# Optimization experiments

Measured on AMD Instinct MI355X. Metric: run time of the kernel, lower is better.

Reference implementation:

```python
import jax, jax.numpy as jnp
import numpy as np

V, E, H, NL, B, T = 32000, 256, 256, 2, 32, 256


def setup_inputs() -> dict:
    key = jax.random.key(0)
    ks = jax.random.split(key, 20)
    s = 0.05
    d = {}
    d['x'] = jax.random.randint(ks[0], (B, T), 0, V)
    d['encoder_output'] = jax.random.normal(ks[1], (T + 1, B, 2 * H), jnp.float32)
    d['encoder_final_state'] = jax.random.normal(ks[2], (2 * NL, B, H), jnp.float32)
    d['embedding'] = jax.random.normal(ks[3], (V, E), jnp.float32) * s
    d['enc_proj_w'] = jax.random.normal(ks[4], (H, 2 * H), jnp.float32) * s
    d['enc_proj_b'] = jnp.zeros((H,), jnp.float32)
    d['attn_wq'] = jax.random.normal(ks[5], (H, H), jnp.float32) * s
    d['attn_wk'] = jax.random.normal(ks[6], (H, H), jnp.float32) * s
    d['attn_wv'] = jax.random.normal(ks[7], (H,), jnp.float32) * s
    d['gru_w_ih0'] = jax.random.normal(ks[8], (3 * H, E + H), jnp.float32) * s
    d['gru_w_hh0'] = jax.random.normal(ks[9], (3 * H, H), jnp.float32) * s
    d['gru_b_ih0'] = jnp.zeros((3 * H,), jnp.float32)
    d['gru_b_hh0'] = jnp.zeros((3 * H,), jnp.float32)
    d['gru_w_ih1'] = jax.random.normal(ks[10], (3 * H, H), jnp.float32) * s
    d['gru_w_hh1'] = jax.random.normal(ks[11], (3 * H, H), jnp.float32) * s
    d['gru_b_ih1'] = jnp.zeros((3 * H,), jnp.float32)
    d['gru_b_hh1'] = jnp.zeros((3 * H,), jnp.float32)
    d['dense_w'] = jax.random.normal(ks[12], (V, H), jnp.float32) * s
    d['dense_b'] = jnp.zeros((V,), jnp.float32)
    return d


def _gru_cell(xin, h, w_ih, w_hh, b_ih, b_hh):
    gi = xin @ w_ih.T + b_ih
    gh = h @ w_hh.T + b_hh
    i_r, i_z, i_n = jnp.split(gi, 3, axis=-1)
    h_r, h_z, h_n = jnp.split(gh, 3, axis=-1)
    r = jax.nn.sigmoid(i_r + h_r)
    z = jax.nn.sigmoid(i_z + h_z)
    n = jnp.tanh(i_n + r * h_n)
    return (1.0 - z) * n + z * h


def _forward(x, encoder_output, encoder_final_state, embedding, enc_proj_w, enc_proj_b,
             attn_wq, attn_wk, attn_wv,
             gru_w_ih0, gru_w_hh0, gru_b_ih0, gru_b_hh0,
             gru_w_ih1, gru_w_hh1, gru_b_ih1, gru_b_hh1,
             dense_w, dense_b):
    Bb, Tt = x.shape
    Hh = enc_proj_w.shape[0]
    L = 2 * Tt  # fixed KV buffer length (= max attention width)
    # project encoder output: (B, T+1, H)
    proj = jnp.einsum('sbd,hd->bsh', encoder_output, enc_proj_w) + enc_proj_b
    # sum forward/backward encoder final states -> (n_layers, B, H)
    h0 = encoder_final_state.reshape(NL, 2, Bb, Hh).sum(axis=1)
    emb = embedding[x].transpose(1, 0, 2)  # (T, B, E)
    # fixed-size KV buffer; slots [0, T+1) hold projected encoder output
    kv0 = jnp.zeros((Bb, L, Hh), proj.dtype).at[:, :Tt + 1, :].set(proj)
    kproj0 = jnp.einsum('blh,gh->blg', kv0, attn_wk)  # precomputed key projections

    def step(carry, inp):
        h, kv, kproj = carry
        emb_t, t = inp
        q = h[-1] @ attn_wq.T  # (B, H)
        scores = jnp.tanh(kproj + q[:, None, :]) @ attn_wv  # (B, L)
        valid = jnp.arange(L) < (Tt + 1 + t)
        attn = jax.nn.softmax(jnp.where(valid[None, :], scores, -1e9), axis=-1)
        attn = attn * valid[None, :].astype(attn.dtype)  # exact zeros at padding
        context = jnp.einsum('bl,blh->bh', attn, kv)
        xin = jnp.concatenate([context, emb_t], axis=-1)  # (B, H+E)
        h0n = _gru_cell(xin, h[0], gru_w_ih0, gru_w_hh0, gru_b_ih0, gru_b_hh0)
        h1n = _gru_cell(h0n, h[1], gru_w_ih1, gru_w_hh1, gru_b_ih1, gru_b_hh1)
        h_new = jnp.stack([h0n, h1n], axis=0)
        out = h1n  # top-layer output for this timestep
        pos = Tt + 1 + t
        kv = jax.lax.dynamic_update_slice_in_dim(kv, out[:, None, :], pos, axis=1)
        kproj = jax.lax.dynamic_update_slice_in_dim(kproj, (out @ attn_wk.T)[:, None, :], pos, axis=1)
        return (h_new, kv, kproj), (out, attn)

    (_, _, _), (outs, attns) = jax.lax.scan(step, (h0, kv0, kproj0), (emb, jnp.arange(Tt)))
    outs = outs.transpose(1, 0, 2)  # (B, T, H)
    logits = jnp.einsum('bth,vh->btv', outs, dense_w) + dense_b  # (B, T, V)
    attn_scores = attns.transpose(1, 0, 2)  # (B, T, 2T)
    return logits, attn_scores


def reference(x, encoder_output, encoder_final_state, embedding, enc_proj_w, enc_proj_b,
              attn_wq, attn_wk, attn_wv,
              gru_w_ih0, gru_w_hh0, gru_b_ih0, gru_b_hh0,
              gru_w_ih1, gru_w_hh1, gru_b_ih1, gru_b_hh1,
              dense_w, dense_b):
    return _forward(x, encoder_output, encoder_final_state, embedding, enc_proj_w, enc_proj_b,
                    attn_wq, attn_wk, attn_wv,
                    gru_w_ih0, gru_w_hh0, gru_b_ih0, gru_b_hh0,
                    gru_w_ih1, gru_w_hh1, gru_b_ih1, gru_b_hh1,
                    dense_w, dense_b)
```

## Files before the change

kernel.cpp:

```cpp
#include <hip/hip_runtime.h>
#include <hip/hip_bf16.h>
#include <hip/hip_fp16.h>

#define NB 32
#define NT 256
#define NH 256
#define NV 32000
#define NL2 512
#define NTP1 257

typedef unsigned int u32x4 __attribute__((ext_vector_type(4)));
typedef unsigned int u32x2 __attribute__((ext_vector_type(2)));
typedef short s16x8 __attribute__((ext_vector_type(8)));
typedef float f32x4 __attribute__((ext_vector_type(4)));
typedef _Float16 half2v __attribute__((ext_vector_type(2)));

#define AGENT __HIP_MEMORY_SCOPE_AGENT
__device__ __forceinline__ float aload(const float* p) {
  return __hip_atomic_load((float*)p, __ATOMIC_RELAXED, AGENT);
}
__device__ __forceinline__ void astore(float* p, float v) {
  __hip_atomic_store(p, v, __ATOMIC_RELAXED, AGENT);
}

__device__ __forceinline__ float dot2f(half2v a, half2v b, float c) {
#if __has_builtin(__builtin_amdgcn_fdot2)
  return __builtin_amdgcn_fdot2(a, b, c, false);
#else
  return c + (float)a[0] * (float)b[0] + (float)a[1] * (float)b[1];
#endif
}
__device__ __forceinline__ half2v h2(unsigned int u) { return __builtin_bit_cast(half2v, u); }

__device__ __forceinline__ float dot16h(const _Float16* __restrict__ w,
                                        const _Float16* __restrict__ x) {
  u32x4 a0 = *(const u32x4*)w;
  u32x4 a1 = *(const u32x4*)(w + 8);
  u32x4 b0 = *(const u32x4*)x;
  u32x4 b1 = *(const u32x4*)(x + 8);
  float acc = 0.f;
  acc = dot2f(h2(a0.x), h2(b0.x), acc);
  acc = dot2f(h2(a0.y), h2(b0.y), acc);
  acc = dot2f(h2(a0.z), h2(b0.z), acc);
  acc = dot2f(h2(a0.w), h2(b0.w), acc);
  acc = dot2f(h2(a1.x), h2(b1.x), acc);
  acc = dot2f(h2(a1.y), h2(b1.y), acc);
  acc = dot2f(h2(a1.z), h2(b1.z), acc);
  acc = dot2f(h2(a1.w), h2(b1.w), acc);
  return acc;
}

__device__ __forceinline__ float fast_tanh(float x) {
  x = fminf(15.f, fmaxf(-15.f, x));
  float e = __expf(2.f * x);
  return 1.f - __fdividef(2.f, e + 1.f);
}
__device__ __forceinline__ float fast_sigmoid(float x) {
  x = fminf(30.f, fmaxf(-30.f, x));
  float e = __expf(-x);
  return __fdividef(1.f, 1.f + e);
}
__device__ __forceinline__ unsigned short f2bf(float f) {
  unsigned int u = __builtin_bit_cast(unsigned int, f);
  return (unsigned short)((u + 0x7FFFu + ((u >> 16) & 1u)) >> 16);
}

__device__ __forceinline__ void batch_barrier(int* __restrict__ ctr, int target) {
  __syncthreads();
  if (threadIdx.x == 0) {
    __hip_atomic_fetch_add(ctr, 1, __ATOMIC_RELEASE, AGENT);
    while (__hip_atomic_load(ctr, __ATOMIC_RELAXED, AGENT) < target)
      __builtin_amdgcn_s_sleep(1);
    asm volatile("" ::: "memory");
  }
  __syncthreads();
}


__global__ void conv_f16_kernel(const float* __restrict__ s, _Float16* __restrict__ d, int n) {
  int i = blockIdx.x * 256 + threadIdx.x;
  if (i < n) d[i] = (_Float16)s[i];
}

__global__ void conv_bf16_kernel(const float* __restrict__ s, unsigned short* __restrict__ d, int n) {
  int i = blockIdx.x * 256 + threadIdx.x;
  if (i < n) d[i] = f2bf(s[i]);
}

__global__ void packT_kernel(const float* __restrict__ w, unsigned int* __restrict__ out,
                             int R, int K) {
  int gid = blockIdx.x * 256 + threadIdx.x;
  int K2 = K >> 1;
  if (gid >= R * K2) return;
  int k2 = gid / R, r = gid - k2 * R;
  unsigned short ua = __builtin_bit_cast(unsigned short, (_Float16)w[(size_t)r * K + 2 * k2]);
  unsigned short ub = __builtin_bit_cast(unsigned short, (_Float16)w[(size_t)r * K + 2 * k2 + 1]);
  out[(size_t)k2 * R + r] = (unsigned int)ua | ((unsigned int)ub << 16);
}

__global__ void transpose_kernel(const float* __restrict__ w, float* __restrict__ wT) {
  int i = blockIdx.x * 256 + threadIdx.x;
  if (i < 256 * 512) { int h = i >> 9, dd = i & 511; wT[dd * 256 + h] = w[i]; }
}
// ... 48 lines not shown
      float kvv = (float)kvL[((size_t)b * 512 + l) * 256 + h];
#pragma unroll
      for (int g = 0; g < 32; ++g) acc[g] = fmaf(kvv, wks[g][h], acc[g]);
    }
    for (int g = 0; g < 32; ++g)
      kprojL[((size_t)b * NL2 + l) * NH + gq * 32 + g] = (_Float16)acc[g];
  }
  {
    int g = tid >> 3, hc = tid & 7;
    float acc = 0.f;
    for (int h = hc * 32; h < hc * 32 + 32; ++h)
      acc += (float)kvL[((size_t)b * 512 + 256) * 256 + h] * wks[g][h];
    pk[g][hc] = acc;
    __syncthreads();
    if (tid < 32) {
      float sv = 0.f;
      for (int c = 0; c < 8; ++c) sv += pk[tid][c];
      kprojL[((size_t)b * NL2 + 256) * NH + gq * 32 + tid] = (_Float16)sv;
    }
  }
}


__global__ __launch_bounds__(512) void scan_kernel(
    const int* __restrict__ x, const float* __restrict__ efs, const float* __restrict__ emb,
    const float* __restrict__ wv,
    const float* __restrict__ bih0, const float* __restrict__ bhh0,
    const float* __restrict__ bih1, const float* __restrict__ bhh1,
    const _Float16* __restrict__ wq16, const _Float16* __restrict__ wk16,
    const unsigned int* __restrict__ wih0T, const unsigned int* __restrict__ whh0T,
    const unsigned int* __restrict__ wih1T, const unsigned int* __restrict__ whh1T,
    const unsigned int* __restrict__ kvL_u, const unsigned int* __restrict__ kprojL_u,
    float* __restrict__ spart, float* __restrict__ vec0, float* __restrict__ vec1,
    int* __restrict__ bars,
    unsigned short* __restrict__ outs_bf, float* __restrict__ attn_out) {
  __shared__ __align__(16) unsigned int kp_u[512 * 17];
  __shared__ __align__(16) unsigned int kv_u[512 * 19];
  __shared__ __align__(16) float att[512], gsum[1024];
  __shared__ __align__(16) float h0s[256], h1s[256];
  __shared__ __align__(16) float scr[544], scr2[32 * 35];
  __shared__ __align__(16) float qs[32], wvs[32], red[16];
  __shared__ __align__(16) _Float16 h0h[256], h1h[256], xinh[64];

  int tid = threadIdx.x;
  int b = blockIdx.x & 31;
  int s = blockIdx.x >> 5;
  int* bar = bars + b * 32;

  if (tid < 256) {
    float h0v = efs[(size_t)(0 * NB + b) * NH + tid] + efs[(size_t)(1 * NB + b) * NH + tid];
    float h1v = efs[(size_t)(2 * NB + b) * NH + tid] + efs[(size_t)(3 * NB + b) * NH + tid];
    h0s[tid] = h0v; h0h[tid] = (_Float16)h0v;
    h1s[tid] = h1v; h1h[tid] = (_Float16)h1v;
  }
  if (tid < 32) wvs[tid] = wv[32 * s + tid];
  for (int idx = tid; idx < 257 * 16; idx += 512) {
    int l = idx >> 4, c = idx & 15;
    kp_u[l * 17 + c] = kprojL_u[((size_t)b * 512 + l) * 128 + 16 * s + c];
    kv_u[l * 19 + c] = kvL_u[((size_t)b * 512 + l) * 128 + 16 * s + c];
  }
  for (int idx = tid; idx < 255 * 16; idx += 512) {
    int l = 257 + (idx >> 4), c = idx & 15;
    kp_u[l * 17 + c] = 0u;
    kv_u[l * 19 + c] = 0u;
  }
  __syncthreads();

  for (int t = 0; t < NT; ++t) {
    int Lt = NTP1 + t;
    int tgt = 8 * (t + 1);
    {
      int row = tid & 31, ch = tid >> 5;
      scr[ch * 33 + row] = dot16h(wq16 + (size_t)(32 * s + row) * 256 + ch * 16, h1h + ch * 16);
      if (tid >= 480) {
        int j = tid - 480;
        int tok = x[b * NT + t];
        xinh[32 + j] = (_Float16)emb[(size_t)tok * 256 + 32 * s + j];
      }
    }
    __syncthreads();
    if (tid < 32) {
      float a = 0.f;
#pragma unroll
      for (int c = 0; c < 16; ++c) a += scr[c * 33 + tid];
      qs[tid] = a;
    }
    __syncthreads();
    {
      float acc = 0.f;
      if (tid < Lt) {
        const unsigned int* kr = kp_u + tid * 17;
#pragma unroll 4
        for (int g2 = 0; g2 < 16; ++g2) {
          half2v kp2 = h2(kr[g2]);
          acc = fmaf(wvs[2 * g2 + 0], fast_tanh((float)kp2[0] + qs[2 * g2 + 0]), acc);
          acc = fmaf(wvs[2 * g2 + 1], fast_tanh((float)kp2[1] + qs[2 * g2 + 1]), acc);
        }
      }
      astore(spart + ((size_t)(b * 8 + s)) * 512 + tid, acc);
    }
    batch_barrier(bar + 0, tgt);
    {
      float sum = 0.f;
#pragma unroll
      for (int sp = 0; sp < 8; ++sp) sum += aload(spart + ((size_t)(b * 8 + sp)) * 512 + tid);
      float v = (tid < Lt) ? sum : -3.0e38f;
      float m = v;
#pragma unroll
      for (int off = 32; off; off >>= 1) m = fmaxf(m, __shfl_xor(m, off, 64));
      if ((tid & 63) == 0) red[tid >> 6] = m;
      __syncthreads();
      float M = red[0];
#pragma unroll
      for (int i = 1; i < 8; ++i) M = fmaxf(M, red[i]);
      float e = (tid < Lt) ? __expf(v - M) : 0.f;
      float zz = e;
#pragma unroll
      for (int off = 32; off; off >>= 1) zz += __shfl_xor(zz, off, 64);
      if ((tid & 63) == 0) red[8 + (tid >> 6)] = zz;
      __syncthreads();
      float Z = red[8];
#pragma unroll
      for (int i = 1; i < 8; ++i) Z += red[8 + i];
      float a = __fdividef(e, Z);
      att[tid] = a;
      if ((tid >> 6) == s) attn_out[((size_t)(b * NT + t)) * NL2 + tid] = a;
    }
    __syncthreads();
    {
      int c = tid >> 4, hh = tid & 15;
      float aA = 0.f, aB = 0.f;
#pragma unroll
      for (int j = 0; j < 16; ++j) {
        int l = 16 * c + j;
        half2v kv2 = h2(kv_u[l * 19 + hh]);
        float av = att[l];
        aA = fmaf((float)kv2[0], av, aA);
        aB = fmaf((float)kv2[1], av, aB);
      }
      scr2[c * 35 + 2 * hh] = aA;
      scr2[c * 35 + 2 * hh + 1] = aB;
    }
    __syncthreads();
    if (tid < 32) {
      float a = 0.f;
#pragma unroll
      for (int c = 0; c < 32; ++c) a += scr2[c * 35 + tid];
      xinh[tid] = (_Float16)a;
    }
    __syncthreads();
    {
      const unsigned int* xu = (const unsigned int*)xinh;
      const unsigned int* h0u = (const unsigned int*)h0h;
      float accA = 0.f, accI = 0.f, accH = 0.f;
      bool dual = (tid < 256);
#pragma unroll 2
      for (int i = 0; i < 16; ++i) {
        unsigned int xc = xu[i], xe = xu[16 + i];
        const unsigned int* wc = wih0T + (size_t)(16 * s + i) * 768;
        const unsigned int* we = wih0T + (size_t)(128 + 16 * s + i) * 768;
        accA = dot2f(h2(wc[tid]), h2(xc), accA);
        accA = dot2f(h2(we[tid]), h2(xe), accA);
        if (dual) {
          accI = dot2f(h2(wc[512 + tid]), h2(xc), accI);
          accI = dot2f(h2(we[512 + tid]), h2(xe), accI);
        }
      }
#pragma unroll 2
      for (int i = 0; i < 16; ++i) {
        unsigned int hv = h0u[16 * s + i];
        const unsigned int* wr = whh0T + (size_t)(16 * s + i) * 768;
        accA = dot2f(h2(wr[tid]), h2(hv), accA);
        if (dual) accH = dot2f(h2(wr[512 + tid]), h2(hv), accH);
      }
      float* vb = vec0 + (size_t)(b * 8 + s) * 1024;
      astore(vb + tid, accA);
      if (dual) { astore(vb + 512 + tid, accI); astore(vb + 768 + tid, accH); }
    }
    batch_barrier(bar + 1, tgt);
    {
      float t0 = 0.f, t1 = 0.f;
#pragma unroll
      for (int sp = 0; sp < 8; ++sp) {
        const float* vb = vec0 + (size_t)(b * 8 + sp) * 1024;
        t0 += aload(vb + tid);
        t1 += aload(vb + 512 + tid);
      }
      gsum[tid] = t0; gsum[512 + tid] = t1;
    }
    __syncthreads();
    if (tid < 256) {
      float rr = fast_sigmoid(gsum[tid] + bih0[tid] + bhh0[tid]);
      float zz = fast_sigmoid(gsum[256 + tid] + bih0[256 + tid] + bhh0[256 + tid]);
      float nn = fast_tanh(gsum[512 + tid] + bih0[512 + tid] + rr * (gsum[768 + tid] + bhh0[512 + tid]));
      float hv = (1.f - zz) * nn + zz * h0s[tid];
      h0s[tid] = hv; h0h[tid] = (_Float16)hv;
    }
    __syncthreads();
    {
      const unsigned int* h0u = (const unsigned int*)h0h;
      const unsigned int* h1u = (const unsigned int*)h1h;
      float accA = 0.f, accI = 0.f, accH = 0.f;
      bool dual = (tid < 256);
#pragma unroll 2
      for (int i = 0; i < 16; ++i) {
        unsigned int xv = h0u[16 * s + i];
        unsigned int hv = h1u[16 * s + i];
        const unsigned int* wi = wih1T + (size_t)(16 * s + i) * 768;
        const unsigned int* wh = whh1T + (size_t)(16 * s + i) * 768;
        accA = dot2f(h2(wi[tid]), h2(xv), accA);
        accA = dot2f(h2(wh[tid]), h2(hv), accA);
        if (dual) {
          accI = dot2f(h2(wi[512 + tid]), h2(xv), accI);
          accH = dot2f(h2(wh[512 + tid]), h2(hv), accH);
        }
      }
      float* vb = vec1 + (size_t)(b * 8 + s) * 1024;
      astore(vb + tid, accA);
      if (dual) { astore(vb + 512 + tid, accI); astore(vb + 768 + tid, accH); }
    }
    batch_barrier(bar + 2, tgt);
    {
      float t0 = 0.f, t1 = 0.f;
#pragma unroll
      for (int sp = 0; sp < 8; ++sp) {
        const float* vb = vec1 + (size_t)(b * 8 + sp) * 1024;
        t0 += aload(vb + tid);
        t1 += aload(vb + 512 + tid);
      }
      gsum[tid] = t0; gsum[512 + tid] = t1;
    }
    __syncthreads();
    if (tid < 256) {
      float rr = fast_sigmoid(gsum[tid] + bih1[tid] + bhh1[tid]);
      float zz = fast_sigmoid(gsum[256 + tid] + bih1[256 + tid] + bhh1[256 + tid]);
      float nn = fast_tanh(gsum[512 + tid] + bih1[512 + tid] + rr * (gsum[768 + tid] + bhh1[512 + tid]));
      float hv = (1.f - zz) * nn + zz * h1s[tid];
      h1s[tid] = hv; h1h[tid] = (_Float16)hv;
      if ((tid >> 5) == s) outs_bf[((size_t)(b * NT + t)) * NH + tid] = f2bf(hv);
    }
    __syncthreads();
    if (t < NT - 1) {
      int pos = NTP1 + t;
      if (tid < 16) {
        unsigned short lo = __builtin_bit_cast(unsigned short, h1h[32 * s + 2 * tid]);
        unsigned short hi = __builtin_bit_cast(unsigned short, h1h[32 * s + 2 * tid + 1]);
        kv_u[pos * 19 + tid] = (unsigned int)lo | ((unsigned int)hi << 16);
      }
      {
        int row = tid & 31, ch = tid >> 5;
        scr[ch * 33 + row] = dot16h(wk16 + (size_t)(32 * s + row) * 256 + ch * 16, h1h + ch * 16);
      }
      __syncthreads();
      if (tid < 32) {
        float a = 0.f;
#pragma unroll
        for (int c = 0; c < 16; ++c) a += scr[c * 33 + tid];
        ((_Float16*)kp_u)[pos * 34 + tid] = (_Float16)a;
      }
      __syncthreads();
    }
  }
}


__global__ __launch_bounds__(256) void logits_gemm(const unsigned short* __restrict__ A,
                                                   const unsigned short* __restrict__ Bw,
                                                   const float* __restrict__ bias,
                                                   float* __restrict__ C) {
  __shared__ unsigned short As[128][88];
  __shared__ unsigned short Bs[128][88];
  int tid = threadIdx.x;
  int nt = blockIdx.x % 250, mt = blockIdx.x / 250;
  int m0 = mt * 128, n0 = nt * 128;
  int lane = tid & 63, w = tid >> 6;
  int wm = w & 1, wn = w >> 1;
  f32x4 acc[4][4];
#pragma unroll
  for (int m = 0; m < 4; ++m)
#pragma unroll
    for (int n = 0; n < 4; ++n) acc[m][n] = (f32x4)0.0f;

  int r0 = tid >> 3;
  int c0 = (tid & 7) * 8;
  for (int kt = 0; kt < 4; ++kt) {
    __syncthreads();
#pragma unroll
    for (int it = 0; it < 4; ++it) {
      int row = it * 32 + r0;
      u32x4 va = *(const u32x4*)(A + (size_t)(m0 + row) * 256 + kt * 64 + c0);
      u32x4 vb = *(const u32x4*)(Bw + (size_t)(n0 + row) * 256 + kt * 64 + c0);
      *(u32x4*)(&As[row][c0]) = va;
      *(u32x4*)(&Bs[row][c0]) = vb;
    }
// ... 35 lines not shown
  const int*   x    = (const int*)d_in[0];
  const float* enc  = (const float*)d_in[1];
  const float* efs  = (const float*)d_in[2];
  const float* emb  = (const float*)d_in[3];
  const float* epw  = (const float*)d_in[4];
  const float* epb  = (const float*)d_in[5];
  const float* wq   = (const float*)d_in[6];
  const float* wk   = (const float*)d_in[7];
  const float* wv   = (const float*)d_in[8];
  const float* wih0 = (const float*)d_in[9];
  const float* whh0 = (const float*)d_in[10];
  const float* bih0 = (const float*)d_in[11];
  const float* bhh0 = (const float*)d_in[12];
  const float* wih1 = (const float*)d_in[13];
  const float* whh1 = (const float*)d_in[14];
  const float* bih1 = (const float*)d_in[15];
  const float* bhh1 = (const float*)d_in[16];
  const float* dw   = (const float*)d_in[17];
  const float* db   = (const float*)d_in[18];

  const size_t o_alias  = 0;
  const size_t a_wq16   = 0;
  const size_t a_wk16   = a_wq16 + 131072;
  const size_t a_wih0T  = a_wk16 + 131072;
  const size_t a_whh0T  = a_wih0T + 786432;
  const size_t a_wih1T  = a_whh0T + 393216;
  const size_t a_whh1T  = a_wih1T + 393216;
  const size_t a_kvL    = a_whh1T + 393216;
  const size_t o_wT     = o_alias + 16384000;
  const size_t o_kprojL = o_wT + 524288;
  const size_t o_outs   = o_kprojL + 8388608;
  const size_t o_spart  = o_outs + 4194304;
  const size_t o_vec0   = o_spart + 524288;
  const size_t o_vec1   = o_vec0 + 1048576;
  const size_t o_bar    = o_vec1 + 1048576;
  const size_t need     = o_bar + 4096;
  if (ws_size < need) return;

  char* ws = (char*)d_ws;
  unsigned short* dwbf16 = (unsigned short*)(ws + o_alias);
  _Float16* wq16     = (_Float16*)(ws + a_wq16);
  _Float16* wk16     = (_Float16*)(ws + a_wk16);
  unsigned int* wih0T = (unsigned int*)(ws + a_wih0T);
  unsigned int* whh0T = (unsigned int*)(ws + a_whh0T);
  unsigned int* wih1T = (unsigned int*)(ws + a_wih1T);
  unsigned int* whh1T = (unsigned int*)(ws + a_whh1T);
  _Float16* kvL      = (_Float16*)(ws + a_kvL);
  float* wT          = (float*)(ws + o_wT);
  _Float16* kprojL   = (_Float16*)(ws + o_kprojL);
  unsigned short* outs_bf = (unsigned short*)(ws + o_outs);
  float* spart       = (float*)(ws + o_spart);
  float* vec0        = (float*)(ws + o_vec0);
  float* vec1        = (float*)(ws + o_vec1);
  int* bars          = (int*)(ws + o_bar);

  float* logits = (float*)d_out;
  float* attn_out = logits + (size_t)NB * NT * NV;

  hipMemsetAsync(ws + o_bar, 0, 4096, stream);

  conv_f16_kernel<<<(65536 + 255) / 256, 256, 0, stream>>>(wq, wq16, 65536);
  conv_f16_kernel<<<(65536 + 255) / 256, 256, 0, stream>>>(wk, wk16, 65536);
  packT_kernel<<<(768 * 256 + 255) / 256, 256, 0, stream>>>(wih0, wih0T, 768, 512);
  packT_kernel<<<(768 * 128 + 255) / 256, 256, 0, stream>>>(whh0, whh0T, 768, 256);
  packT_kernel<<<(768 * 128 + 255) / 256, 256, 0, stream>>>(wih1, wih1T, 768, 256);
  packT_kernel<<<(768 * 128 + 255) / 256, 256, 0, stream>>>(whh1, whh1T, 768, 256);
  transpose_kernel<<<(131072 + 255) / 256, 256, 0, stream>>>(epw, wT);

  proj_kernel<<<(NTP1 * NB * 64) / 256, 256, 0, stream>>>(enc, wT, epb, kvL);
  kproj0_kernel<<<NB * 8, 256, 0, stream>>>(kvL, wk, kprojL);

  scan_kernel<<<256, 512, 0, stream>>>(x, efs, emb, wv, bih0, bhh0, bih1, bhh1,
                                       wq16, wk16, wih0T, whh0T, wih1T, whh1T,
                                       (const unsigned int*)kvL, (const unsigned int*)kprojL,
                                       spart, vec0, vec1, bars,
                                       outs_bf, attn_out);

  conv_bf16_kernel<<<(8192000 + 255) / 256, 256, 0, stream>>>(dw, dwbf16, 8192000);

  logits_gemm<<<(NB * NT / 128) * (NV / 128), 256, 0, stream>>>(outs_bf, dwbf16, db, logits);
}
```

Before: 7.129 ms.

## Split grid barriers into arrive/wait and overlap hidden-state matvecs with barrier waits

Splits the cross-block barrier into arrive and wait phases. Independent work runs in the gap: both layers' W_hh·h matvecs after the attention-score barrier, the attention output store, and prefetching the next token's embedding. The partial-sum buffers become double-buffered by timestep parity and widened to hold separate input and hidden contributions, which avoids overwrite races now that writes move earlier. The aim is to hide barrier latency on the serial recurrence. The cost is larger workspace and more global partial loads in the reductions.

```diff
diff --git a/kernel.cpp b/kernel.cpp
--- a/kernel.cpp
+++ b/kernel.cpp
@@ -65,10 +65,13 @@
   return (unsigned short)((u + 0x7FFFu + ((u >> 16) & 1u)) >> 16);
 }
 
-__device__ __forceinline__ void batch_barrier(int* __restrict__ ctr, int target) {
+__device__ __forceinline__ void bar_arrive(int* __restrict__ ctr) {
   __syncthreads();
+  if (threadIdx.x == 0)
+    __hip_atomic_fetch_add(ctr, 1, __ATOMIC_RELEASE, AGENT);
+}
+__device__ __forceinline__ void bar_wait(int* __restrict__ ctr, int target) {
   if (threadIdx.x == 0) {
-    __hip_atomic_fetch_add(ctr, 1, __ATOMIC_RELEASE, AGENT);
     while (__hip_atomic_load(ctr, __ATOMIC_RELAXED, AGENT) < target)
       __builtin_amdgcn_s_sleep(1);
     asm volatile("" ::: "memory");
@@ -205,6 +208,11 @@
     h1s[tid] = h1v; h1h[tid] = (_Float16)h1v;
   }
   if (tid < 32) wvs[tid] = wv[32 * s + tid];
+  if (tid >= 480) {
+    int j = tid - 480;
+    int tok = x[b * NT + 0];
+    xinh[32 + j] = (_Float16)emb[(size_t)tok * 256 + 32 * s + j];
+  }
   for (int idx = tid; idx < 257 * 16; idx += 512) {
     int l = idx >> 4, c = idx & 15;
     kp_u[l * 17 + c] = kprojL_u[((size_t)b * 512 + l) * 128 + 16 * s + c];
@@ -220,14 +228,11 @@
   for (int t = 0; t < NT; ++t) {
     int Lt = NTP1 + t;
     int tgt = 8 * (t + 1);
+    int buf = t & 1;
+    const size_t vbase = ((size_t)(buf * NB + b)) * 8;
     {
       int row = tid & 31, ch = tid >> 5;
       scr[ch * 33 + row] = dot16h(wq16 + (size_t)(32 * s + row) * 256 + ch * 16, h1h + ch * 16);
-      if (tid >= 480) {
-        int j = tid - 480;
-        int tok = x[b * NT + t];
-        xinh[32 + j] = (_Float16)emb[(size_t)tok * 256 + 32 * s + j];
-      }
     }
     __syncthreads();
     if (tid < 32) {
@@ -250,7 +255,32 @@
       }
       astore(spart + ((size_t)(b * 8 + s)) * 512 + tid, acc);
     }
-    batch_barrier(bar + 0, tgt);
+    bar_arrive(bar + 0);
+    {
+      const unsigned int* h0u = (const unsigned int*)h0h;
+      const unsigned int* h1u = (const unsigned int*)h1h;
+      float a0v = 0.f, a0d = 0.f, a1v = 0.f, a1d = 0.f;
+      bool dual = (tid < 256);
+#pragma unroll 4
+      for (int i = 0; i < 16; ++i) {
+        unsigned int hv0 = h0u[16 * s + i];
+        unsigned int hv1 = h1u[16 * s + i];
+        const unsigned int* w0r = whh0T + (size_t)(16 * s + i) * 768;
+        const unsigned int* w1r = whh1T + (size_t)(16 * s + i) * 768;
+        a0v = dot2f(h2(w0r[tid]), h2(hv0), a0v);
+        a1v = dot2f(h2(w1r[tid]), h2(hv1), a1v);
+        if (dual) {
+          a0d = dot2f(h2(w0r[512 + tid]), h2(hv0), a0d);
+          a1d = dot2f(h2(w1r[512 + tid]), h2(hv1), a1d);
+        }
+      }
+      float* v0 = vec0 + (vbase + s) * 1536 + 768;
+      float* v1 = vec1 + (vbase + s) * 1536 + 768;
+      astore(v0 + tid, a0v);
+      astore(v1 + tid, a1v);
+      if (dual) { astore(v0 + 512 + tid, a0d); astore(v1 + 512 + tid, a1d); }
+    }
+    bar_wait(bar + 0, tgt);
     {
       float sum = 0.f;
 #pragma unroll
@@ -273,9 +303,7 @@
       float Z = red[8];
 #pragma unroll
       for (int i = 1; i < 8; ++i) Z += red[8 + i];
-      float a = __fdividef(e, Z);
-      att[tid] = a;
-      if ((tid >> 6) == s) attn_out[((size_t)(b * NT + t)) * NL2 + tid] = a;
+      att[tid] = __fdividef(e, Z);
     }
     __syncthreads();
     {
@@ -302,42 +330,47 @@
     __syncthreads();
     {
       const unsigned int* xu = (const unsigned int*)xinh;
-      const unsigned int* h0u = (const unsigned int*)h0h;
-      float accA = 0.f, accI = 0.f, accH = 0.f;
+      float g1 = 0.f, g2 = 0.f;
       bool dual = (tid < 256);
-#pragma unroll 2
+#pragma unroll 4
       for (int i = 0; i < 16; ++i) {
         unsigned int xc = xu[i], xe = xu[16 + i];
         const unsigned int* wc = wih0T + (size_t)(16 * s + i) * 768;
         const unsigned int* we = wih0T + (size_t)(128 + 16 * s + i) * 768;
-        accA = dot2f(h2(wc[tid]), h2(xc), accA);
-        accA = dot2f(h2(we[tid]), h2(xe), accA);
+        g1 = dot2f(h2(wc[tid]), h2(xc), g1);
+        g1 = dot2f(h2(we[tid]), h2(xe), g1);
         if (dual) {
-          accI = dot2f(h2(wc[512 + tid]), h2(xc), accI);
-          accI = dot2f(h2(we[512 + tid]), h2(xe), accI);
+          g2 = dot2f(h2(wc[512 + tid]), h2(xc), g2);
+          g2 = dot2f(h2(we[512 + tid]), h2(xe), g2);
         }
       }
-#pragma unroll 2
-      for (int i = 0; i < 16; ++i) {
-        unsigned int hv = h0u[16 * s + i];
-        const unsigned int* wr = whh0T + (size_t)(16 * s + i) * 768;
-        accA = dot2f(h2(wr[tid]), h2(hv), accA);
-        if (dual) accH = dot2f(h2(wr[512 + tid]), h2(hv), accH);
-      }
-      float* vb = vec0 + (size_t)(b * 8 + s) * 1024;
-      astore(vb + tid, accA);
-      if (dual) { astore(vb + 512 + tid, accI); astore(vb + 768 + tid, accH); }
-    }
-    batch_barrier(bar + 1, tgt);
-    {
-      float t0 = 0.f, t1 = 0.f;
+      float* vb = vec0 + (vbase + s) * 1536;
+      astore(vb + tid, g1);
+      if (dual) astore(vb + 512 + tid, g2);
+    }
+    bar_arrive(bar + 1);
+    if ((tid >> 6) == s) attn_out[((size_t)(b * NT + t)) * NL2 + tid] = att[tid];
+    bar_wait(bar + 1, tgt);
+    {
+      float t0 = 0.f;
 #pragma unroll
       for (int sp = 0; sp < 8; ++sp) {
-        const float* vb = vec0 + (size_t)(b * 8 + sp) * 1024;
-        t0 += aload(vb + tid);
-        t1 += aload(vb + 512 + tid);
-      }
-      gsum[tid] = t0; gsum[512 + tid] = t1;
+        const float* vb = vec0 + (vbase + sp) * 1536;
+        t0 += aload(vb + tid) + aload(vb + 768 + tid);
+      }
+      gsum[tid] = t0;
+      if (tid < 256) {
+        float ti = 0.f;
+#pragma unroll
+        for (int sp = 0; sp < 8; ++sp) ti += aload(vec0 + (vbase + sp) * 1536 + 512 + tid);
+        gsum[512 + tid] = ti;
+      } else {
+        int j = tid - 256;
+        float th = 0.f;
+#pragma unroll
+        for (int sp = 0; sp < 8; ++sp) th += aload(vec0 + (vbase + sp) * 1536 + 1280 + j);
+        gsum[768 + j] = th;
+      }
     }
     __syncthreads();
     if (tid < 256) {
@@ -350,36 +383,46 @@
     __syncthreads();
     {
       const unsigned int* h0u = (const unsigned int*)h0h;
-      const unsigned int* h1u = (const unsigned int*)h1h;
-      float accA = 0.f, accI = 0.f, accH = 0.f;
+      float g1 = 0.f, g2 = 0.f;
       bool dual = (tid < 256);
-#pragma unroll 2
+#pragma unroll 4
       for (int i = 0; i < 16; ++i) {
         unsigned int xv = h0u[16 * s + i];
-        unsigned int hv = h1u[16 * s + i];
         const unsigned int* wi = wih1T + (size_t)(16 * s + i) * 768;
-        const unsigned int* wh = whh1T + (size_t)(16 * s + i) * 768;
-        accA = dot2f(h2(wi[tid]), h2(xv), accA);
-        accA = dot2f(h2(wh[tid]), h2(hv), accA);
-        if (dual) {
-          accI = dot2f(h2(wi[512 + tid]), h2(xv), accI);
-          accH = dot2f(h2(wh[512 + tid]), h2(hv), accH);
-        }
-      }
-      float* vb = vec1 + (size_t)(b * 8 + s) * 1024;
-      astore(vb + tid, accA);
-      if (dual) { astore(vb + 512 + tid, accI); astore(vb + 768 + tid, accH); }
-    }
-    batch_barrier(bar + 2, tgt);
-    {
-      float t0 = 0.f, t1 = 0.f;
+        g1 = dot2f(h2(wi[tid]), h2(xv), g1);
+        if (dual) g2 = dot2f(h2(wi[512 + tid]), h2(xv), g2);
+      }
+      float* vb = vec1 + (vbase + s) * 1536;
+      astore(vb + tid, g1);
+      if (dual) astore(vb + 512 + tid, g2);
+    }
+    bar_arrive(bar + 2);
+    if (t < NT - 1 && tid >= 480) {
+      int j = tid - 480;
+      int tok = x[b * NT + t + 1];
+      xinh[32 + j] = (_Float16)emb[(size_t)tok * 256 + 32 * s + j];
+    }
+    bar_wait(bar + 2, tgt);
+    {
+      float t0 = 0.f;
 #pragma unroll
       for (int sp = 0; sp < 8; ++sp) {
-        const float* vb = vec1 + (size_t)(b * 8 + sp) * 1024;
-        t0 += aload(vb + tid);
-        t1 += aload(vb + 512 + tid);
-      }
-      gsum[tid] = t0; gsum[512 + tid] = t1;
+        const float* vb = vec1 + (vbase + sp) * 1536;
+        t0 += aload(vb + tid) + aload(vb + 768 + tid);
+      }
+      gsum[tid] = t0;
+      if (tid < 256) {
+        float ti = 0.f;
+#pragma unroll
+        for (int sp = 0; sp < 8; ++sp) ti += aload(vec1 + (vbase + sp) * 1536 + 512 + tid);
+        gsum[512 + tid] = ti;
+      } else {
+        int j = tid - 256;
+        float th = 0.f;
+#pragma unroll
+        for (int sp = 0; sp < 8; ++sp) th += aload(vec1 + (vbase + sp) * 1536 + 1280 + j);
+        gsum[768 + j] = th;
+      }
     }
     __syncthreads();
     if (tid < 256) {
@@ -512,8 +555,8 @@
   const size_t o_outs   = o_kprojL + 8388608;
   const size_t o_spart  = o_outs + 4194304;
   const size_t o_vec0   = o_spart + 524288;
-  const size_t o_vec1   = o_vec0 + 1048576;
-  const size_t o_bar    = o_vec1 + 1048576;
+  const size_t o_vec1   = o_vec0 + 3145728;
+  const size_t o_bar    = o_vec1 + 3145728;
   const size_t need     = o_bar + 4096;
   if (ws_size < need) return;
 
```

Result: slower. 7.278 ms (+2.1%).

## Use XCC-local coherent loads for cross-block reductions when blocks share an XCC

Applied to the files above, without the earlier changes.

At scan-kernel start, each block records its hardware XCC id and waits at a one-time barrier with the other blocks of its batch. It then checks whether all eight blocks of that batch sit on the same XCC. If they do, partial-sum exchanges use plain stores and batched sc0 global loads instead of agent-scope atomic loads and stores. The aim is to cut the latency of the three per-timestep inter-block reductions by keeping that traffic in the shared L2 rather than in device-coherent memory. The embedding fetch for the next token also moves to the end of the previous step, taking it off the critical path, and the slower atomic path stays as a fallback when placement differs.

```diff
diff --git a/kernel.cpp b/kernel.cpp
--- a/kernel.cpp
+++ b/kernel.cpp
@@ -21,6 +21,43 @@
 }
 __device__ __forceinline__ void astore(float* p, float v) {
   __hip_atomic_store(p, v, __ATOMIC_RELAXED, AGENT);
+}
+__device__ __forceinline__ unsigned int aloadu(const unsigned int* p) {
+  return __hip_atomic_load((unsigned int*)p, __ATOMIC_RELAXED, AGENT);
+}
+
+__device__ __forceinline__ float sum8_sc0(const float* p, int stride_f) {
+  const float *p1 = p + stride_f, *p2 = p + 2 * stride_f, *p3 = p + 3 * stride_f;
+  const float *p4 = p + 4 * stride_f, *p5 = p + 5 * stride_f;
+  const float *p6 = p + 6 * stride_f, *p7 = p + 7 * stride_f;
+  float v0, v1, v2, v3, v4, v5, v6, v7;
+  asm volatile(
+      "global_load_dword %0, %8, off sc0\n\t"
+      "global_load_dword %1, %9, off sc0\n\t"
+      "global_load_dword %2, %10, off sc0\n\t"
+      "global_load_dword %3, %11, off sc0\n\t"
+      "global_load_dword %4, %12, off sc0\n\t"
+      "global_load_dword %5, %13, off sc0\n\t"
+      "global_load_dword %6, %14, off sc0\n\t"
+      "global_load_dword %7, %15, off sc0\n\t"
+      "s_waitcnt vmcnt(0)"
+      : "=&v"(v0), "=&v"(v1), "=&v"(v2), "=&v"(v3),
+        "=&v"(v4), "=&v"(v5), "=&v"(v6), "=&v"(v7)
+      : "v"(p), "v"(p1), "v"(p2), "v"(p3), "v"(p4), "v"(p5), "v"(p6), "v"(p7)
+      : "memory");
+  return ((v0 + v1) + (v2 + v3)) + ((v4 + v5) + (v6 + v7));
+}
+__device__ __forceinline__ float sum8_agent(const float* p, int stride_f) {
+  float a = 0.f;
+#pragma unroll
+  for (int sp = 0; sp < 8; ++sp) a += aload(p + sp * stride_f);
+  return a;
+}
+__device__ __forceinline__ float sum8x(const float* p, int stride_f, int fastf) {
+  return fastf ? sum8_sc0(p, stride_f) : sum8_agent(p, stride_f);
+}
+__device__ __forceinline__ void xstore(float* p, float v, int fastf) {
+  if (fastf) *p = v; else astore(p, v);
 }
 
 __device__ __forceinline__ float dot2f(half2v a, half2v b, float c) {
@@ -65,7 +102,7 @@
   return (unsigned short)((u + 0x7FFFu + ((u >> 16) & 1u)) >> 16);
 }
 
-__device__ __forceinline__ void batch_barrier(int* __restrict__ ctr, int target) {
+__device__ __forceinline__ void bar_step(int* __restrict__ ctr, int target) {
   __syncthreads();
   if (threadIdx.x == 0) {
     __hip_atomic_fetch_add(ctr, 1, __ATOMIC_RELEASE, AGENT);
@@ -183,7 +220,7 @@
     const unsigned int* __restrict__ wih1T, const unsigned int* __restrict__ whh1T,
     const unsigned int* __restrict__ kvL_u, const unsigned int* __restrict__ kprojL_u,
     float* __restrict__ spart, float* __restrict__ vec0, float* __restrict__ vec1,
-    int* __restrict__ bars,
+    int* __restrict__ bars, unsigned int* __restrict__ xcc_tbl,
     unsigned short* __restrict__ outs_bf, float* __restrict__ attn_out) {
   __shared__ __align__(16) unsigned int kp_u[512 * 17];
   __shared__ __align__(16) unsigned int kv_u[512 * 19];
@@ -205,6 +242,11 @@
     h1s[tid] = h1v; h1h[tid] = (_Float16)h1v;
   }
   if (tid < 32) wvs[tid] = wv[32 * s + tid];
+  if (tid >= 480) {
+    int j = tid - 480;
+    int tok = x[b * NT + 0];
+    xinh[32 + j] = (_Float16)emb[(size_t)tok * 256 + 32 * s + j];
+  }
   for (int idx = tid; idx < 257 * 16; idx += 512) {
     int l = idx >> 4, c = idx & 15;
     kp_u[l * 17 + c] = kprojL_u[((size_t)b * 512 + l) * 128 + 16 * s + c];
@@ -215,6 +257,28 @@
     kp_u[l * 17 + c] = 0u;
     kv_u[l * 19 + c] = 0u;
   }
+
+  int fastf;
+  {
+    if (tid == 0) {
+      unsigned int xid;
+      asm volatile("s_getreg_b32 %0, hwreg(HW_REG_XCC_ID)" : "=s"(xid));
+      __hip_atomic_store(xcc_tbl + blockIdx.x, xid + 1u, __ATOMIC_RELAXED, AGENT);
+    }
+    __syncthreads();
+    if (tid == 0) {
+      __hip_atomic_fetch_add(bar + 8, 1, __ATOMIC_RELEASE, AGENT);
+      while (__hip_atomic_load(bar + 8, __ATOMIC_RELAXED, AGENT) < 8)
+        __builtin_amdgcn_s_sleep(1);
+      asm volatile("" ::: "memory");
+      unsigned int x0 = aloadu(xcc_tbl + b);
+      int ok = (x0 != 0u);
+      for (int sp = 1; sp < 8; ++sp) ok &= (aloadu(xcc_tbl + sp * 32 + b) == x0);
+      red[0] = ok ? 1.f : 0.f;
+    }
+    __syncthreads();
+    fastf = (red[0] != 0.f) ? 1 : 0;
+  }
   __syncthreads();
 
   for (int t = 0; t < NT; ++t) {
@@ -223,11 +287,6 @@
     {
       int row = tid & 31, ch = tid >> 5;
       scr[ch * 33 + row] = dot16h(wq16 + (size_t)(32 * s + row) * 256 + ch * 16, h1h + ch * 16);
-      if (tid >= 480) {
-        int j = tid - 480;
-        int tok = x[b * NT + t];
-        xinh[32 + j] = (_Float16)emb[(size_t)tok * 256 + 32 * s + j];
-      }
     }
     __syncthreads();
     if (tid < 32) {
@@ -248,13 +307,11 @@
           acc = fmaf(wvs[2 * g2 + 1], fast_tanh((float)kp2[1] + qs[2 * g2 + 1]), acc);
         }
       }
-      astore(spart + ((size_t)(b * 8 + s)) * 512 + tid, acc);
-    }
-    batch_barrier(bar + 0, tgt);
-    {
-      float sum = 0.f;
-#pragma unroll
-      for (int sp = 0; sp < 8; ++sp) sum += aload(spart + ((size_t)(b * 8 + sp)) * 512 + tid);
+      xstore(spart + ((size_t)(b * 8 + s)) * 512 + tid, acc, fastf);
+    }
+    bar_step(bar + 0, tgt);
+    {
+      float sum = sum8x(spart + (size_t)b * 8 * 512 + tid, 512, fastf);
       float v = (tid < Lt) ? sum : -3.0e38f;
       float m = v;
 #pragma unroll
@@ -325,19 +382,14 @@
         if (dual) accH = dot2f(h2(wr[512 + tid]), h2(hv), accH);
       }
       float* vb = vec0 + (size_t)(b * 8 + s) * 1024;
-      astore(vb + tid, accA);
-      if (dual) { astore(vb + 512 + tid, accI); astore(vb + 768 + tid, accH); }
-    }
-    batch_barrier(bar + 1, tgt);
-    {
-      float t0 = 0.f, t1 = 0.f;
-#pragma unroll
-      for (int sp = 0; sp < 8; ++sp) {
-        const float* vb = vec0 + (size_t)(b * 8 + sp) * 1024;
-        t0 += aload(vb + tid);
-        t1 += aload(vb + 512 + tid);
-      }
-      gsum[tid] = t0; gsum[512 + tid] = t1;
+      xstore(vb + tid, accA, fastf);
+      if (dual) { xstore(vb + 512 + tid, accI, fastf); xstore(vb + 768 + tid, accH, fastf); }
+    }
+    bar_step(bar + 1, tgt);
+    {
+      const float* vb0 = vec0 + (size_t)b * 8 * 1024;
+      gsum[tid] = sum8x(vb0 + tid, 1024, fastf);
+      gsum[512 + tid] = sum8x(vb0 + 512 + tid, 1024, fastf);
     }
     __syncthreads();
     if (tid < 256) {
@@ -367,19 +419,14 @@
         }
       }
       float* vb = vec1 + (size_t)(b * 8 + s) * 1024;
-      astore(vb + tid, accA);
-      if (dual) { astore(vb + 512 + tid, accI); astore(vb + 768 + tid, accH); }
-    }
-    batch_barrier(bar + 2, tgt);
-    {
-      float t0 = 0.f, t1 = 0.f;
-#pragma unroll
-      for (int sp = 0; sp < 8; ++sp) {
-        const float* vb = vec1 + (size_t)(b * 8 + sp) * 1024;
-        t0 += aload(vb + tid);
-        t1 += aload(vb + 512 + tid);
-      }
-      gsum[tid] = t0; gsum[512 + tid] = t1;
+      xstore(vb + tid, accA, fastf);
+      if (dual) { xstore(vb + 512 + tid, accI, fastf); xstore(vb + 768 + tid, accH, fastf); }
+    }
+    bar_step(bar + 2, tgt);
+    {
+      const float* vb1 = vec1 + (size_t)b * 8 * 1024;
+      gsum[tid] = sum8x(vb1 + tid, 1024, fastf);
+      gsum[512 + tid] = sum8x(vb1 + 512 + tid, 1024, fastf);
     }
     __syncthreads();
     if (tid < 256) {
@@ -408,6 +455,11 @@
 #pragma unroll
         for (int c = 0; c < 16; ++c) a += scr[c * 33 + tid];
         ((_Float16*)kp_u)[pos * 34 + tid] = (_Float16)a;
+      }
+      if (tid >= 480) {
+        int j = tid - 480;
+        int tok = x[b * NT + t + 1];
+        xinh[32 + j] = (_Float16)emb[(size_t)tok * 256 + 32 * s + j];
       }
       __syncthreads();
     }
@@ -514,7 +566,8 @@
   const size_t o_vec0   = o_spart + 524288;
   const size_t o_vec1   = o_vec0 + 1048576;
   const size_t o_bar    = o_vec1 + 1048576;
-  const size_t need     = o_bar + 4096;
+  const size_t o_xcc    = o_bar + 4096;
+  const size_t need     = o_xcc + 1024;
   if (ws_size < need) return;
 
   char* ws = (char*)d_ws;
@@ -533,11 +586,12 @@
   float* vec0        = (float*)(ws + o_vec0);
   float* vec1        = (float*)(ws + o_vec1);
   int* bars          = (int*)(ws + o_bar);
+  unsigned int* xcc_tbl = (unsigned int*)(ws + o_xcc);
 
   float* logits = (float*)d_out;
   float* attn_out = logits + (size_t)NB * NT * NV;
 
-  hipMemsetAsync(ws + o_bar, 0, 4096, stream);
+  hipMemsetAsync(ws + o_bar, 0, 5120, stream);
 
   conv_f16_kernel<<<(65536 + 255) / 256, 256, 0, stream>>>(wq, wq16, 65536);
   conv_f16_kernel<<<(65536 + 255) / 256, 256, 0, stream>>>(wk, wk16, 65536);
@@ -553,7 +607,7 @@
   scan_kernel<<<256, 512, 0, stream>>>(x, efs, emb, wv, bih0, bhh0, bih1, bhh1,
                                        wq16, wk16, wih0T, whh0T, wih1T, whh1T,
                                        (const unsigned int*)kvL, (const unsigned int*)kprojL,
-                                       spart, vec0, vec1, bars,
+                                       spart, vec0, vec1, bars, xcc_tbl,
                                        outs_bf, attn_out);
 
   conv_bf16_kernel<<<(8192000 + 255) / 256, 256, 0, stream>>>(dw, dwbf16, 8192000);
```

Result: slower. 7.652 ms (+7.3%).

## Interleave two batch elements per scan block to hide cross-block barrier latency

Applied to the files above, without the earlier changes.

Each scan block now processes two batch elements (b and b+16) instead of one, and the grid shrinks from 256 to 128 blocks. The cross-block barrier is split into separate arrive and wait steps, and the phases of the two elements are interleaved, so one element's compute can run while the other's barrier is pending. The embedding fetch for the next step is also prefetched at the end of the current step. In exchange, each block does twice the serial work per step and LDS use roughly doubles (kv padding drops from 19 to 17), which may hurt latency or bank behavior.

```diff
diff --git a/kernel.cpp b/kernel.cpp
--- a/kernel.cpp
+++ b/kernel.cpp
@@ -10,7 +10,6 @@
 #define NTP1 257
 
 typedef unsigned int u32x4 __attribute__((ext_vector_type(4)));
-typedef unsigned int u32x2 __attribute__((ext_vector_type(2)));
 typedef short s16x8 __attribute__((ext_vector_type(8)));
 typedef float f32x4 __attribute__((ext_vector_type(4)));
 typedef _Float16 half2v __attribute__((ext_vector_type(2)));
@@ -21,6 +20,12 @@
 }
 __device__ __forceinline__ void astore(float* p, float v) {
   __hip_atomic_store(p, v, __ATOMIC_RELAXED, AGENT);
+}
+__device__ __forceinline__ float sum8_agent(const float* p, int stride_f) {
+  float a = 0.f;
+#pragma unroll
+  for (int sp = 0; sp < 8; ++sp) a += aload(p + sp * stride_f);
+  return a;
 }
 
 __device__ __forceinline__ float dot2f(half2v a, half2v b, float c) {
@@ -65,10 +70,13 @@
   return (unsigned short)((u + 0x7FFFu + ((u >> 16) & 1u)) >> 16);
 }
 
-__device__ __forceinline__ void batch_barrier(int* __restrict__ ctr, int target) {
+__device__ __forceinline__ void bar_arrive(int* __restrict__ ctr) {
   __syncthreads();
+  if (threadIdx.x == 0)
+    __hip_atomic_fetch_add(ctr, 1, __ATOMIC_RELEASE, AGENT);
+}
+__device__ __forceinline__ void bar_wait(int* __restrict__ ctr, int target) {
   if (threadIdx.x == 0) {
-    __hip_atomic_fetch_add(ctr, 1, __ATOMIC_RELEASE, AGENT);
     while (__hip_atomic_load(ctr, __ATOMIC_RELAXED, AGENT) < target)
       __builtin_amdgcn_s_sleep(1);
     asm volatile("" ::: "memory");
@@ -185,76 +193,82 @@
     float* __restrict__ spart, float* __restrict__ vec0, float* __restrict__ vec1,
     int* __restrict__ bars,
     unsigned short* __restrict__ outs_bf, float* __restrict__ attn_out) {
-  __shared__ __align__(16) unsigned int kp_u[512 * 17];
-  __shared__ __align__(16) unsigned int kv_u[512 * 19];
-  __shared__ __align__(16) float att[512], gsum[1024];
-  __shared__ __align__(16) float h0s[256], h1s[256];
-  __shared__ __align__(16) float scr[544], scr2[32 * 35];
-  __shared__ __align__(16) float qs[32], wvs[32], red[16];
-  __shared__ __align__(16) _Float16 h0h[256], h1h[256], xinh[64];
+  __shared__ __align__(16) unsigned int kp_u[2][512 * 17];
+  __shared__ __align__(16) unsigned int kv_u[2][512 * 17];
+  __shared__ __align__(16) float h0s[2][256], h1s[2][256], att[2][512], qs[2][32];
+  __shared__ __align__(16) _Float16 h0h[2][256], h1h[2][256], xinh[2][64];
+  __shared__ __align__(16) float gsum[1024], scr[544], scr2[32 * 35], wvs[32], red[16];
 
   int tid = threadIdx.x;
-  int b = blockIdx.x & 31;
-  int s = blockIdx.x >> 5;
-  int* bar = bars + b * 32;
-
-  if (tid < 256) {
-    float h0v = efs[(size_t)(0 * NB + b) * NH + tid] + efs[(size_t)(1 * NB + b) * NH + tid];
-    float h1v = efs[(size_t)(2 * NB + b) * NH + tid] + efs[(size_t)(3 * NB + b) * NH + tid];
-    h0s[tid] = h0v; h0h[tid] = (_Float16)h0v;
-    h1s[tid] = h1v; h1h[tid] = (_Float16)h1v;
-  }
+  int w = blockIdx.x;
+  int s = w >> 4;
+  int bA = w & 15;
+  int bb[2] = {bA, bA + 16};
+
   if (tid < 32) wvs[tid] = wv[32 * s + tid];
-  for (int idx = tid; idx < 257 * 16; idx += 512) {
-    int l = idx >> 4, c = idx & 15;
-    kp_u[l * 17 + c] = kprojL_u[((size_t)b * 512 + l) * 128 + 16 * s + c];
-    kv_u[l * 19 + c] = kvL_u[((size_t)b * 512 + l) * 128 + 16 * s + c];
-  }
-  for (int idx = tid; idx < 255 * 16; idx += 512) {
-    int l = 257 + (idx >> 4), c = idx & 15;
-    kp_u[l * 17 + c] = 0u;
-    kv_u[l * 19 + c] = 0u;
+#pragma unroll
+  for (int cx = 0; cx < 2; ++cx) {
+    int b = bb[cx];
+    if (tid < 256) {
+      float h0v = efs[(size_t)(0 * NB + b) * NH + tid] + efs[(size_t)(1 * NB + b) * NH + tid];
+      float h1v = efs[(size_t)(2 * NB + b) * NH + tid] + efs[(size_t)(3 * NB + b) * NH + tid];
+      h0s[cx][tid] = h0v; h0h[cx][tid] = (_Float16)h0v;
+      h1s[cx][tid] = h1v; h1h[cx][tid] = (_Float16)h1v;
+    }
+    if (tid >= 480) {
+      int j = tid - 480;
+      int tok = x[b * NT + 0];
+      xinh[cx][32 + j] = (_Float16)emb[(size_t)tok * 256 + 32 * s + j];
+    }
+    for (int idx = tid; idx < 257 * 16; idx += 512) {
+      int l = idx >> 4, c = idx & 15;
+      kp_u[cx][l * 17 + c] = kprojL_u[((size_t)b * 512 + l) * 128 + 16 * s + c];
+      kv_u[cx][l * 17 + c] = kvL_u[((size_t)b * 512 + l) * 128 + 16 * s + c];
+    }
+    for (int idx = tid; idx < 255 * 16; idx += 512) {
+      int l = 257 + (idx >> 4), c = idx & 15;
+      kp_u[cx][l * 17 + c] = 0u;
+      kv_u[cx][l * 17 + c] = 0u;
+    }
   }
   __syncthreads();
 
-  for (int t = 0; t < NT; ++t) {
-    int Lt = NTP1 + t;
-    int tgt = 8 * (t + 1);
+  auto P12 = [&](int cx, int Lt) {
+    int b = bb[cx];
     {
       int row = tid & 31, ch = tid >> 5;
-      scr[ch * 33 + row] = dot16h(wq16 + (size_t)(32 * s + row) * 256 + ch * 16, h1h + ch * 16);
-      if (tid >= 480) {
-        int j = tid - 480;
-        int tok = x[b * NT + t];
-        xinh[32 + j] = (_Float16)emb[(size_t)tok * 256 + 32 * s + j];
-      }
+      scr[ch * 33 + row] = dot16h(wq16 + (size_t)(32 * s + row) * 256 + ch * 16,
+                                  h1h[cx] + ch * 16);
     }
     __syncthreads();
     if (tid < 32) {
       float a = 0.f;
 #pragma unroll
       for (int c = 0; c < 16; ++c) a += scr[c * 33 + tid];
-      qs[tid] = a;
+      qs[cx][tid] = a;
     }
     __syncthreads();
     {
       float acc = 0.f;
       if (tid < Lt) {
-        const unsigned int* kr = kp_u + tid * 17;
+        const unsigned int* kr = kp_u[cx] + tid * 17;
 #pragma unroll 4
         for (int g2 = 0; g2 < 16; ++g2) {
           half2v kp2 = h2(kr[g2]);
-          acc = fmaf(wvs[2 * g2 + 0], fast_tanh((float)kp2[0] + qs[2 * g2 + 0]), acc);
-          acc = fmaf(wvs[2 * g2 + 1], fast_tanh((float)kp2[1] + qs[2 * g2 + 1]), acc);
+          acc = fmaf(wvs[2 * g2 + 0], fast_tanh((float)kp2[0] + qs[cx][2 * g2 + 0]), acc);
+          acc = fmaf(wvs[2 * g2 + 1], fast_tanh((float)kp2[1] + qs[cx][2 * g2 + 1]), acc);
         }
       }
       astore(spart + ((size_t)(b * 8 + s)) * 512 + tid, acc);
     }
-    batch_barrier(bar + 0, tgt);
-    {
-      float sum = 0.f;
-#pragma unroll
-      for (int sp = 0; sp < 8; ++sp) sum += aload(spart + ((size_t)(b * 8 + sp)) * 512 + tid);
+    bar_arrive(bars + b * 32 + 0);
+  };
+
+  auto SCG = [&](int cx, int t, int Lt, int tgt) {
+    int b = bb[cx];
+    bar_wait(bars + b * 32 + 0, tgt);
+    {
+      float sum = sum8_agent(spart + (size_t)b * 8 * 512 + tid, 512);
       float v = (tid < Lt) ? sum : -3.0e38f;
       float m = v;
 #pragma unroll
@@ -274,7 +288,7 @@
 #pragma unroll
       for (int i = 1; i < 8; ++i) Z += red[8 + i];
       float a = __fdividef(e, Z);
-      att[tid] = a;
+      att[cx][tid] = a;
       if ((tid >> 6) == s) attn_out[((size_t)(b * NT + t)) * NL2 + tid] = a;
     }
     __syncthreads();
@@ -284,8 +298,8 @@
 #pragma unroll
       for (int j = 0; j < 16; ++j) {
         int l = 16 * c + j;
-        half2v kv2 = h2(kv_u[l * 19 + hh]);
-        float av = att[l];
+        half2v kv2 = h2(kv_u[cx][l * 17 + hh]);
+        float av = att[cx][l];
         aA = fmaf((float)kv2[0], av, aA);
         aB = fmaf((float)kv2[1], av, aB);
       }
@@ -297,12 +311,12 @@
       float a = 0.f;
 #pragma unroll
       for (int c = 0; c < 32; ++c) a += scr2[c * 35 + tid];
-      xinh[tid] = (_Float16)a;
-    }
-    __syncthreads();
-    {
-      const unsigned int* xu = (const unsigned int*)xinh;
-      const unsigned int* h0u = (const unsigned int*)h0h;
+      xinh[cx][tid] = (_Float16)a;
+    }
+    __syncthreads();
+    {
+      const unsigned int* xu = (const unsigned int*)xinh[cx];
+      const unsigned int* h0u = (const unsigned int*)h0h[cx];
       float accA = 0.f, accI = 0.f, accH = 0.f;
       bool dual = (tid < 256);
 #pragma unroll 2
@@ -328,29 +342,29 @@
       astore(vb + tid, accA);
       if (dual) { astore(vb + 512 + tid, accI); astore(vb + 768 + tid, accH); }
     }
-    batch_barrier(bar + 1, tgt);
-    {
-      float t0 = 0.f, t1 = 0.f;
-#pragma unroll
-      for (int sp = 0; sp < 8; ++sp) {
-        const float* vb = vec0 + (size_t)(b * 8 + sp) * 1024;
-        t0 += aload(vb + tid);
-        t1 += aload(vb + 512 + tid);
-      }
-      gsum[tid] = t0; gsum[512 + tid] = t1;
+    bar_arrive(bars + b * 32 + 1);
+  };
+
+  auto CG1 = [&](int cx, int tgt) {
+    int b = bb[cx];
+    bar_wait(bars + b * 32 + 1, tgt);
+    {
+      const float* vb0 = vec0 + (size_t)b * 8 * 1024;
+      gsum[tid] = sum8_agent(vb0 + tid, 1024);
+      gsum[512 + tid] = sum8_agent(vb0 + 512 + tid, 1024);
     }
     __syncthreads();
     if (tid < 256) {
       float rr = fast_sigmoid(gsum[tid] + bih0[tid] + bhh0[tid]);
       float zz = fast_sigmoid(gsum[256 + tid] + bih0[256 + tid] + bhh0[256 + tid]);
       float nn = fast_tanh(gsum[512 + tid] + bih0[512 + tid] + rr * (gsum[768 + tid] + bhh0[512 + tid]));
-      float hv = (1.f - zz) * nn + zz * h0s[tid];
-      h0s[tid] = hv; h0h[tid] = (_Float16)hv;
-    }
-    __syncthreads();
-    {
-      const unsigned int* h0u = (const unsigned int*)h0h;
-      const unsigned int* h1u = (const unsigned int*)h1h;
+      float hv = (1.f - zz) * nn + zz * h0s[cx][tid];
+      h0s[cx][tid] = hv; h0h[cx][tid] = (_Float16)hv;
+    }
+    __syncthreads();
+    {
+      const unsigned int* h0u = (const unsigned int*)h0h[cx];
+      const unsigned int* h1u = (const unsigned int*)h1h[cx];
       float accA = 0.f, accI = 0.f, accH = 0.f;
       bool dual = (tid < 256);
 #pragma unroll 2
@@ -370,47 +384,62 @@
       astore(vb + tid, accA);
       if (dual) { astore(vb + 512 + tid, accI); astore(vb + 768 + tid, accH); }
     }
-    batch_barrier(bar + 2, tgt);
-    {
-      float t0 = 0.f, t1 = 0.f;
-#pragma unroll
-      for (int sp = 0; sp < 8; ++sp) {
-        const float* vb = vec1 + (size_t)(b * 8 + sp) * 1024;
-        t0 += aload(vb + tid);
-        t1 += aload(vb + 512 + tid);
-      }
-      gsum[tid] = t0; gsum[512 + tid] = t1;
+    bar_arrive(bars + b * 32 + 2);
+  };
+
+  auto C1A = [&](int cx, int t, int tgt) {
+    int b = bb[cx];
+    bar_wait(bars + b * 32 + 2, tgt);
+    {
+      const float* vb1 = vec1 + (size_t)b * 8 * 1024;
+      gsum[tid] = sum8_agent(vb1 + tid, 1024);
+      gsum[512 + tid] = sum8_agent(vb1 + 512 + tid, 1024);
     }
     __syncthreads();
     if (tid < 256) {
       float rr = fast_sigmoid(gsum[tid] + bih1[tid] + bhh1[tid]);
       float zz = fast_sigmoid(gsum[256 + tid] + bih1[256 + tid] + bhh1[256 + tid]);
       float nn = fast_tanh(gsum[512 + tid] + bih1[512 + tid] + rr * (gsum[768 + tid] + bhh1[512 + tid]));
-      float hv = (1.f - zz) * nn + zz * h1s[tid];
-      h1s[tid] = hv; h1h[tid] = (_Float16)hv;
+      float hv = (1.f - zz) * nn + zz * h1s[cx][tid];
+      h1s[cx][tid] = hv; h1h[cx][tid] = (_Float16)hv;
       if ((tid >> 5) == s) outs_bf[((size_t)(b * NT + t)) * NH + tid] = f2bf(hv);
     }
     __syncthreads();
     if (t < NT - 1) {
       int pos = NTP1 + t;
       if (tid < 16) {
-        unsigned short lo = __builtin_bit_cast(unsigned short, h1h[32 * s + 2 * tid]);
-        unsigned short hi = __builtin_bit_cast(unsigned short, h1h[32 * s + 2 * tid + 1]);
-        kv_u[pos * 19 + tid] = (unsigned int)lo | ((unsigned int)hi << 16);
+        unsigned short lo = __builtin_bit_cast(unsigned short, h1h[cx][32 * s + 2 * tid]);
+        unsigned short hi = __builtin_bit_cast(unsigned short, h1h[cx][32 * s + 2 * tid + 1]);
+        kv_u[cx][pos * 17 + tid] = (unsigned int)lo | ((unsigned int)hi << 16);
       }
       {
         int row = tid & 31, ch = tid >> 5;
-        scr[ch * 33 + row] = dot16h(wk16 + (size_t)(32 * s + row) * 256 + ch * 16, h1h + ch * 16);
+        scr[ch * 33 + row] = dot16h(wk16 + (size_t)(32 * s + row) * 256 + ch * 16,
+                                    h1h[cx] + ch * 16);
       }
       __syncthreads();
       if (tid < 32) {
         float a = 0.f;
 #pragma unroll
         for (int c = 0; c < 16; ++c) a += scr[c * 33 + tid];
-        ((_Float16*)kp_u)[pos * 34 + tid] = (_Float16)a;
+        ((_Float16*)kp_u[cx])[pos * 34 + tid] = (_Float16)a;
+      }
+      if (tid >= 480) {
+        int j = tid - 480;
+        int tok = x[b * NT + t + 1];
+        xinh[cx][32 + j] = (_Float16)emb[(size_t)tok * 256 + 32 * s + j];
       }
       __syncthreads();
     }
+  };
+
+  for (int t = 0; t < NT; ++t) {
+    int Lt = NTP1 + t;
+    int tgt = 8 * (t + 1);
+    P12(0, Lt);        P12(1, Lt);
+    SCG(0, t, Lt, tgt); SCG(1, t, Lt, tgt);
+    CG1(0, tgt);        CG1(1, tgt);
+    C1A(0, t, tgt);     C1A(1, t, tgt);
   }
 }
 
@@ -550,7 +579,7 @@
   proj_kernel<<<(NTP1 * NB * 64) / 256, 256, 0, stream>>>(enc, wT, epb, kvL);
   kproj0_kernel<<<NB * 8, 256, 0, stream>>>(kvL, wk, kprojL);
 
-  scan_kernel<<<256, 512, 0, stream>>>(x, efs, emb, wv, bih0, bhh0, bih1, bhh1,
+  scan_kernel<<<128, 512, 0, stream>>>(x, efs, emb, wv, bih0, bhh0, bih1, bhh1,
                                        wq16, wk16, wih0T, whh0T, wih1T, whh1T,
                                        (const unsigned int*)kvL, (const unsigned int*)kprojL,
                                        spart, vec0, vec1, bars,
```

Result: slower. 10.36 ms (+45.3%).
